# Optimization experiments

Measured on AMD Instinct MI355X. Metric: run time of the kernel, lower is better.

## Reference

```python
import jax, jax.numpy as jnp
import numpy as np

GROUP_SIZES = (64, 128, 256, 96, 160, 224, 192, 288, 320, 112, 80, 48, 32, 16, 32)
LENGTH = 512
ALPHABET = 21


def setup_inputs() -> dict:
    key = jax.random.key(0)
    keys = jax.random.split(key, len(GROUP_SIZES) + 1)
    n_samples = int(sum(GROUP_SIZES))
    inp = {"x": jax.random.normal(keys[0], (n_samples, LENGTH, ALPHABET), dtype=jnp.float32)}
    for i, g in enumerate(GROUP_SIZES):
        inp[f"mat{i}"] = jax.random.normal(keys[i + 1], (g, g), dtype=jnp.float32)
    return inp


def reference(x, mat0, mat1, mat2, mat3, mat4, mat5, mat6, mat7, mat8, mat9,
              mat10, mat11, mat12, mat13, mat14):
    mats = (mat0, mat1, mat2, mat3, mat4, mat5, mat6, mat7, mat8, mat9,
            mat10, mat11, mat12, mat13, mat14)
    # Block-diagonal grouped matmul along the sample dim: out[sl] = mats_i @ x[sl].
    # Group boundaries are static Python ints, so slicing is jit-friendly.
    pieces = []
    start = 0
    for m, g in zip(mats, GROUP_SIZES):
        xg = x[start:start + g]  # (g, L, A)
        pieces.append(jnp.einsum('gh,hla->gla', m, xg))
        start += g
    return jnp.concatenate(pieces, axis=0)
```

## Files before the change

### kernel.cpp

```cpp
#include <hip/hip_runtime.h>
#include <hip/hip_bf16.h>

#define NCOL 10752
#define NROW 2048
#define NG 15
#define NTILES 23

typedef __bf16 bf16;
typedef __attribute__((ext_vector_type(8))) __bf16 bf16x8;
typedef __attribute__((ext_vector_type(4))) __bf16 bf16x4;
typedef __attribute__((ext_vector_type(4))) float f32x4;

__constant__ int c_gsize[NG]  = {64,128,256,96,160,224,192,288,320,112,80,48,32,16,32};
__constant__ int c_gstart[NG] = {0,64,192,448,544,704,928,1120,1408,1728,1840,1920,1968,2000,2016};
__constant__ int c_tgrp[NTILES] = {8,8,8,7,7,7,2,2,5,5,6,6,4,4,1,9,3,10,0,11,12,14,13};
__constant__ int c_trow[NTILES] = {0,128,256,0,128,256,0,128,0,128,0,128,0,128,0,0,0,0,0,0,0,0,0};

struct MatPtrs { const float* p[NG]; };

constexpr int BM = 128, BN = 128, BK = 32, BKp = 40;

__global__ __launch_bounds__(256)
void matapply_kernel(const float* __restrict__ x, MatPtrs mats, float* __restrict__ out)
{
    __shared__ bf16 sA[2][BM][BKp];
    __shared__ bf16 sB[2][BN][BKp];

    const int tid    = threadIdx.x;
    const int colb   = blockIdx.x * BN;
    const int tileid = blockIdx.y;

    const int grp  = c_tgrp[tileid];
    const int row0 = c_trow[tileid];
    const int g    = c_gsize[grp];
    const int s    = c_gstart[grp];
    const float* __restrict__ M = mats.p[grp];

    const int wave = tid >> 6;
    const int lane = tid & 63;
    const int wr   = (wave & 1) * 64;
    const int wc   = (wave >> 1) * 64;
    const int lm   = lane & 15;
    const int kq   = lane >> 4;
    const int kb   = kq * 8;

    const int aK = (tid & 7) * 4;
    const int aR = tid >> 3;
    const int bC = (tid & 31) * 4;
    const int bK = (tid >> 5) * 4;

    const int nIter = (g + BK - 1) / BK;

    f32x4 acc[4][4];
    #pragma unroll
    for (int i = 0; i < 4; i++)
        #pragma unroll
        for (int j = 0; j < 4; j++)
            acc[i][j] = (f32x4){0.f, 0.f, 0.f, 0.f};

    float4 av[4], xv[4];

    #pragma unroll
    for (int i = 0; i < 4; i++) {
        int r = aR + 32 * i;
        av[i] = make_float4(0.f, 0.f, 0.f, 0.f);
        if ((row0 + r) < g && aK < g)
            av[i] = *(const float4*)(M + (size_t)(row0 + r) * g + aK);
    }
    #pragma unroll
    for (int j = 0; j < 4; j++)
        xv[j] = *(const float4*)(x + (size_t)(s + bK + j) * NCOL + colb + bC);

    #pragma unroll
    for (int i = 0; i < 4; i++) {
        int r = aR + 32 * i;
        bf16x4 w;
        w[0] = (bf16)av[i].x; w[1] = (bf16)av[i].y; w[2] = (bf16)av[i].z; w[3] = (bf16)av[i].w;
        *(bf16x4*)&sA[0][r][aK] = w;
    }
    #pragma unroll
    for (int cc = 0; cc < 4; cc++) {
        int lc = bC + cc;
        bf16x4 w;
        #pragma unroll
        for (int j = 0; j < 4; j++)
            w[j] = (bf16)(((const float*)&xv[j])[cc]);
        *(bf16x4*)&sB[0][lc][bK ^ (((lc >> 2) & 3) << 3)] = w;
    }
    __syncthreads();

    for (int it = 0; it < nIter; ++it) {
        const int cur = it & 1;
        const bool more = (it + 1) < nIter;

        if (more) {
            const int k0 = (it + 1) * BK;
            #pragma unroll
            for (int i = 0; i < 4; i++) {
                int r = aR + 32 * i;
                av[i] = make_float4(0.f, 0.f, 0.f, 0.f);
                if ((row0 + r) < g && (k0 + aK) < g)
                    av[i] = *(const float4*)(M + (size_t)(row0 + r) * g + (k0 + aK));
            }
            #pragma unroll
            for (int j = 0; j < 4; j++)
                xv[j] = *(const float4*)(x + (size_t)(s + k0 + bK + j) * NCOL + colb + bC);
        }

        bf16x8 af[4], bfr[4];
        #pragma unroll
        for (int i = 0; i < 4; i++)
            af[i] = *(const bf16x8*)&sA[cur][wr + i * 16 + lm][kb];
        #pragma unroll
        for (int j = 0; j < 4; j++) {
            int lc = wc + j * 16 + lm;
            bfr[j] = *(const bf16x8*)&sB[cur][lc][kb ^ (((lc >> 2) & 3) << 3)];
        }
        #pragma unroll
        for (int i = 0; i < 4; i++)
            #pragma unroll
            for (int j = 0; j < 4; j++)
                acc[i][j] = __builtin_amdgcn_mfma_f32_16x16x32_bf16(af[i], bfr[j], acc[i][j], 0, 0, 0);

        if (more) {
            const int nxt = 1 - cur;
            #pragma unroll
            for (int i = 0; i < 4; i++) {
                int r = aR + 32 * i;
                bf16x4 w;
                w[0] = (bf16)av[i].x; w[1] = (bf16)av[i].y; w[2] = (bf16)av[i].z; w[3] = (bf16)av[i].w;
                *(bf16x4*)&sA[nxt][r][aK] = w;
            }
            #pragma unroll
            for (int cc = 0; cc < 4; cc++) {
                int lc = bC + cc;
                bf16x4 w;
                #pragma unroll
                for (int j = 0; j < 4; j++)
                    w[j] = (bf16)(((const float*)&xv[j])[cc]);
                *(bf16x4*)&sB[nxt][lc][bK ^ (((lc >> 2) & 3) << 3)] = w;
            }
            __syncthreads();
        }
    }

    #pragma unroll
    for (int i = 0; i < 4; i++) {
        #pragma unroll
        for (int r = 0; r < 4; r++) {
            int row = row0 + wr + i * 16 + kq * 4 + r;
            if (row < g) {
                float* orow = out + (size_t)(s + row) * NCOL + colb + wc;
                #pragma unroll
                for (int j = 0; j < 4; j++)
                    orow[j * 16 + lm] = acc[i][j][r];
            }
        }
    }
}

extern "C" void kernel_launch(void* const* d_in, const int* in_sizes, int n_in,
                              void* d_out, int out_size, void* d_ws, size_t ws_size,
                              hipStream_t stream)
{
    const float* x = (const float*)d_in[0];
    MatPtrs mp;
    for (int i = 0; i < NG; i++) mp.p[i] = (const float*)d_in[1 + i];
    float* out = (float*)d_out;

    dim3 grid(NCOL / BN, NTILES);
    dim3 block(256);
    matapply_kernel<<<grid, block, 0, stream>>>(x, mp, out);
}
```

Measured before the change: 192.4 us.

## Shrink GEMM tiles to 64x64 with finer row tiling and new LDS swizzles

Block tiles drop from 128x128 to 64x64, and the row-tile table is rebuilt at 64-row granularity, giving 37 row tiles and a grid four times larger. The aim is less padding waste on groups whose size is not a multiple of 128, plus better occupancy, declared through launch bounds of 6 blocks. New XOR swizzles are applied to the A and B shared-memory tiles to cut bank conflicts. In exchange, each loaded tile is reused across fewer outputs, there are more block launches and barriers per unit of work, and the B stores to shared memory become narrower bf16x2 writes.

```diff
diff --git a/kernel.cpp b/kernel.cpp
--- a/kernel.cpp
+++ b/kernel.cpp
@@ -1,30 +1,36 @@
 #include <hip/hip_runtime.h>
-#include <hip/hip_bf16.h>
 
 #define NCOL 10752
-#define NROW 2048
 #define NG 15
-#define NTILES 23
+#define NTILES 37
 
 typedef __bf16 bf16;
 typedef __attribute__((ext_vector_type(8))) __bf16 bf16x8;
 typedef __attribute__((ext_vector_type(4))) __bf16 bf16x4;
+typedef __attribute__((ext_vector_type(2))) __bf16 bf16x2;
 typedef __attribute__((ext_vector_type(4))) float f32x4;
 
 __constant__ int c_gsize[NG]  = {64,128,256,96,160,224,192,288,320,112,80,48,32,16,32};
 __constant__ int c_gstart[NG] = {0,64,192,448,544,704,928,1120,1408,1728,1840,1920,1968,2000,2016};
-__constant__ int c_tgrp[NTILES] = {8,8,8,7,7,7,2,2,5,5,6,6,4,4,1,9,3,10,0,11,12,14,13};
-__constant__ int c_trow[NTILES] = {0,128,256,0,128,256,0,128,0,128,0,128,0,128,0,0,0,0,0,0,0,0,0};
+__constant__ int c_tgrp[NTILES] = {8,8,8,8,8, 7,7,7,7,7, 2,2,2,2, 5,5,5,5, 6,6,6, 4,4,4, 1,1, 9,9, 3,3, 10,10, 0, 11, 12, 13, 14};
+__constant__ int c_trow[NTILES] = {0,64,128,192,256, 0,64,128,192,256, 0,64,128,192, 0,64,128,192, 0,64,128, 0,64,128, 0,64, 0,64, 0,64, 0,64, 0, 0, 0, 0, 0};
 
 struct MatPtrs { const float* p[NG]; };
 
-constexpr int BM = 128, BN = 128, BK = 32, BKp = 40;
+constexpr int BM = 64, BN = 64, BK = 32, BKp = 40;
 
-__global__ __launch_bounds__(256)
+__device__ __forceinline__ int swzB(int lc, int k) {
+    return k ^ ((((lc >> 2) ^ (lc >> 4)) & 3) << 3);
+}
+__device__ __forceinline__ int swzA(int r, int k) {
+    return k ^ (((r >> 1) & 3) << 3);
+}
+
+__global__ __launch_bounds__(256, 6)
 void matapply_kernel(const float* __restrict__ x, MatPtrs mats, float* __restrict__ out)
 {
-    __shared__ bf16 sA[2][BM][BKp];
-    __shared__ bf16 sB[2][BN][BKp];
+    __shared__ __align__(16) bf16 sA[2][BM][BKp];
+    __shared__ __align__(16) bf16 sB[2][BN][BKp];
 
     const int tid    = threadIdx.x;
     const int colb   = blockIdx.x * BN;
@@ -38,54 +44,53 @@
 
     const int wave = tid >> 6;
     const int lane = tid & 63;
-    const int wr   = (wave & 1) * 64;
-    const int wc   = (wave >> 1) * 64;
+    const int wr   = (wave & 1) * 32;
+    const int wc   = (wave >> 1) * 32;
     const int lm   = lane & 15;
     const int kq   = lane >> 4;
     const int kb   = kq * 8;
 
     const int aK = (tid & 7) * 4;
     const int aR = tid >> 3;
-    const int bC = (tid & 31) * 4;
-    const int bK = (tid >> 5) * 4;
+    const int bC = (tid & 15) * 4;
+    const int bK = (tid >> 4) * 2;
 
     const int nIter = (g + BK - 1) / BK;
 
-    f32x4 acc[4][4];
+    f32x4 acc[2][2];
     #pragma unroll
-    for (int i = 0; i < 4; i++)
+    for (int i = 0; i < 2; i++)
         #pragma unroll
-        for (int j = 0; j < 4; j++)
+        for (int j = 0; j < 2; j++)
             acc[i][j] = (f32x4){0.f, 0.f, 0.f, 0.f};
 
-    float4 av[4], xv[4];
+    float4 av[2], xv[2];
 
     #pragma unroll
-    for (int i = 0; i < 4; i++) {
+    for (int i = 0; i < 2; i++) {
         int r = aR + 32 * i;
         av[i] = make_float4(0.f, 0.f, 0.f, 0.f);
         if ((row0 + r) < g && aK < g)
             av[i] = *(const float4*)(M + (size_t)(row0 + r) * g + aK);
     }
     #pragma unroll
-    for (int j = 0; j < 4; j++)
+    for (int j = 0; j < 2; j++)
         xv[j] = *(const float4*)(x + (size_t)(s + bK + j) * NCOL + colb + bC);
 
     #pragma unroll
-    for (int i = 0; i < 4; i++) {
+    for (int i = 0; i < 2; i++) {
         int r = aR + 32 * i;
         bf16x4 w;
         w[0] = (bf16)av[i].x; w[1] = (bf16)av[i].y; w[2] = (bf16)av[i].z; w[3] = (bf16)av[i].w;
-        *(bf16x4*)&sA[0][r][aK] = w;
+        *(bf16x4*)&sA[0][r][swzA(r, aK)] = w;
     }
     #pragma unroll
     for (int cc = 0; cc < 4; cc++) {
         int lc = bC + cc;
-        bf16x4 w;
-        #pragma unroll
-        for (int j = 0; j < 4; j++)
-            w[j] = (bf16)(((const float*)&xv[j])[cc]);
-        *(bf16x4*)&sB[0][lc][bK ^ (((lc >> 2) & 3) << 3)] = w;
+        bf16x2 w;
+        w[0] = (bf16)(((const float*)&xv[0])[cc]);
+        w[1] = (bf16)(((const float*)&xv[1])[cc]);
+        *(bf16x2*)&sB[0][lc][swzB(lc, bK)] = w;
     }
     __syncthreads();
 
@@ -96,64 +101,64 @@
         if (more) {
             const int k0 = (it + 1) * BK;
             #pragma unroll
-            for (int i = 0; i < 4; i++) {
+            for (int i = 0; i < 2; i++) {
                 int r = aR + 32 * i;
                 av[i] = make_float4(0.f, 0.f, 0.f, 0.f);
                 if ((row0 + r) < g && (k0 + aK) < g)
-                    av[i] = *(const float4*)(M + (size_t)(row0 + r) * g + (k0 + aK));
+                    av[i] = *(const float4*)(M + (size_t)(row0 + r) * g + k0 + aK);
             }
             #pragma unroll
-            for (int j = 0; j < 4; j++)
+            for (int j = 0; j < 2; j++)
                 xv[j] = *(const float4*)(x + (size_t)(s + k0 + bK + j) * NCOL + colb + bC);
         }
 
-        bf16x8 af[4], bfr[4];
+        bf16x8 af[2], bfr[2];
         #pragma unroll
-        for (int i = 0; i < 4; i++)
-            af[i] = *(const bf16x8*)&sA[cur][wr + i * 16 + lm][kb];
-        #pragma unroll
-        for (int j = 0; j < 4; j++) {
-            int lc = wc + j * 16 + lm;
-            bfr[j] = *(const bf16x8*)&sB[cur][lc][kb ^ (((lc >> 2) & 3) << 3)];
+        for (int i = 0; i < 2; i++) {
+            int r = wr + 16 * i + lm;
+            af[i] = *(const bf16x8*)&sA[cur][r][swzA(r, kb)];
         }
         #pragma unroll
-        for (int i = 0; i < 4; i++)
+        for (int j = 0; j < 2; j++) {
+            int lc = wc + 16 * j + lm;
+            bfr[j] = *(const bf16x8*)&sB[cur][lc][swzB(lc, kb)];
+        }
+        #pragma unroll
+        for (int i = 0; i < 2; i++)
             #pragma unroll
-            for (int j = 0; j < 4; j++)
+            for (int j = 0; j < 2; j++)
                 acc[i][j] = __builtin_amdgcn_mfma_f32_16x16x32_bf16(af[i], bfr[j], acc[i][j], 0, 0, 0);
 
         if (more) {
             const int nxt = 1 - cur;
             #pragma unroll
-            for (int i = 0; i < 4; i++) {
+            for (int i = 0; i < 2; i++) {
                 int r = aR + 32 * i;
                 bf16x4 w;
                 w[0] = (bf16)av[i].x; w[1] = (bf16)av[i].y; w[2] = (bf16)av[i].z; w[3] = (bf16)av[i].w;
-                *(bf16x4*)&sA[nxt][r][aK] = w;
+                *(bf16x4*)&sA[nxt][r][swzA(r, aK)] = w;
             }
             #pragma unroll
             for (int cc = 0; cc < 4; cc++) {
                 int lc = bC + cc;
-                bf16x4 w;
-                #pragma unroll
-                for (int j = 0; j < 4; j++)
-                    w[j] = (bf16)(((const float*)&xv[j])[cc]);
-                *(bf16x4*)&sB[nxt][lc][bK ^ (((lc >> 2) & 3) << 3)] = w;
+                bf16x2 w;
+                w[0] = (bf16)(((const float*)&xv[0])[cc]);
+                w[1] = (bf16)(((const float*)&xv[1])[cc]);
+                *(bf16x2*)&sB[nxt][lc][swzB(lc, bK)] = w;
             }
             __syncthreads();
         }
     }
 
     #pragma unroll
-    for (int i = 0; i < 4; i++) {
+    for (int i = 0; i < 2; i++) {
         #pragma unroll
         for (int r = 0; r < 4; r++) {
-            int row = row0 + wr + i * 16 + kq * 4 + r;
+            int row = row0 + wr + 16 * i + kq * 4 + r;
             if (row < g) {
                 float* orow = out + (size_t)(s + row) * NCOL + colb + wc;
-                #pragma unroll
-                for (int j = 0; j < 4; j++)
-                    orow[j * 16 + lm] = acc[i][j][r];
+                orow[lm]      = acc[i][0][r];
+                orow[16 + lm] = acc[i][1][r];
             }
         }
     }
```

Result: slower. 204.0 us (+6.0%).

## Pre-pack weight tiles to bf16 MFMA layout and stream via global_load_lds

Applied to the files above, without the earlier changes.

A new prep kernel converts each group's weight matrix into bf16 tiles laid out in MFMA fragment order in workspace memory. The main kernel then loads the A tiles straight into LDS with global_load_lds, skipping the per-block fp32 load, conversion and LDS writes of the weights. This is meant to cut redundant weight conversion across the 84 column blocks and to ease register pressure (launch bounds now request 4 blocks). The cost is an extra kernel launch and a dependency on workspace size, with the old kernel kept as a fallback.

```diff
diff --git a/kernel.cpp b/kernel.cpp
--- a/kernel.cpp
+++ b/kernel.cpp
@@ -1,10 +1,9 @@
 #include <hip/hip_runtime.h>
-#include <hip/hip_bf16.h>
 
 #define NCOL 10752
-#define NROW 2048
 #define NG 15
 #define NTILES 23
+#define WS_NEED 1064960
 
 typedef __bf16 bf16;
 typedef __attribute__((ext_vector_type(8))) __bf16 bf16x8;
@@ -13,17 +12,48 @@
 
 __constant__ int c_gsize[NG]  = {64,128,256,96,160,224,192,288,320,112,80,48,32,16,32};
 __constant__ int c_gstart[NG] = {0,64,192,448,544,704,928,1120,1408,1728,1840,1920,1968,2000,2016};
-__constant__ int c_tgrp[NTILES] = {8,8,8,7,7,7,2,2,5,5,6,6,4,4,1,9,3,10,0,11,12,14,13};
-__constant__ int c_trow[NTILES] = {0,128,256,0,128,256,0,128,0,128,0,128,0,128,0,0,0,0,0,0,0,0,0};
+__constant__ int c_tgrp[NTILES]  = {8,8,8,7,7,7,2,2,5,5,6,6,4,4,1,9,3,10,0,11,12,14,13};
+__constant__ int c_trow[NTILES]  = {0,128,256,0,128,256,0,128,0,128,0,128,0,128,0,0,0,0,0,0,0,0,0};
+__constant__ int c_niter[NTILES] = {10,10,10,9,9,9,8,8,7,7,6,6,5,5,4,4,3,3,2,2,1,1,1};
+__constant__ int c_tbase[NTILES] = {0,10,20,30,39,48,57,65,73,80,87,93,99,104,109,113,117,120,123,125,127,128,129};
 
 struct MatPtrs { const float* p[NG]; };
 
 constexpr int BM = 128, BN = 128, BK = 32, BKp = 40;
 
 __global__ __launch_bounds__(256)
-void matapply_kernel(const float* __restrict__ x, MatPtrs mats, float* __restrict__ out)
+void prep_kernel(MatPtrs mats, bf16* __restrict__ ws)
 {
-    __shared__ bf16 sA[2][BM][BKp];
+    const int kt = blockIdx.x, tile = blockIdx.y;
+    if (kt >= c_niter[tile]) return;
+    const int grp  = c_tgrp[tile];
+    const int row0 = c_trow[tile];
+    const int g    = c_gsize[grp];
+    const float* __restrict__ M = mats.p[grp];
+    bf16* dst = ws + (size_t)(c_tbase[tile] + kt) * 4096;
+
+    #pragma unroll
+    for (int h = 0; h < 2; h++) {
+        const int u    = threadIdx.x + h * 256;
+        const int l    = u & 63;
+        const int st   = u >> 6;
+        const int row  = row0 + st * 16 + (l & 15);
+        const int kcol = kt * 32 + (l >> 4) * 8;
+        bf16x8 w = {};
+        if (row < g && kcol < g) {
+            const float* src = M + (size_t)row * g + kcol;
+            #pragma unroll
+            for (int j = 0; j < 8; j++) w[j] = (bf16)src[j];
+        }
+        *(bf16x8*)(dst + (size_t)u * 8) = w;
+    }
+}
+
+__global__ __launch_bounds__(256, 4)
+void matapply_kernel(const float* __restrict__ x, const bf16* __restrict__ aws,
+                     float* __restrict__ out)
+{
+    __shared__ bf16 sA[2][4096];
     __shared__ bf16 sB[2][BN][BKp];
 
     const int tid    = threadIdx.x;
@@ -31,10 +61,10 @@
     const int tileid = blockIdx.y;
 
     const int grp  = c_tgrp[tileid];
-    const int row0 = c_trow[tileid];
     const int g    = c_gsize[grp];
     const int s    = c_gstart[grp];
-    const float* __restrict__ M = mats.p[grp];
+    const int row0 = c_trow[tileid];
+    const bf16* __restrict__ aimg = aws + (size_t)c_tbase[tileid] * 4096;
 
     const int wave = tid >> 6;
     const int lane = tid & 63;
@@ -44,6 +74,126 @@
     const int kq   = lane >> 4;
     const int kb   = kq * 8;
 
+    const int bC = (tid & 31) * 4;
+    const int bK = (tid >> 5) * 4;
+
+    const int nIter = (g + BK - 1) / BK;
+
+    f32x4 acc[4][4];
+    #pragma unroll
+    for (int i = 0; i < 4; i++)
+        #pragma unroll
+        for (int j = 0; j < 4; j++)
+            acc[i][j] = (f32x4){0.f, 0.f, 0.f, 0.f};
+
+    float4 xv[4];
+
+    auto glds_a = [&](int buf, int kt) {
+        const bf16* src = aimg + (size_t)kt * 4096 + (size_t)(wave * 2) * 512 + lane * 8;
+        #pragma unroll
+        for (int c = 0; c < 2; c++)
+            __builtin_amdgcn_global_load_lds(
+                (const __attribute__((address_space(1))) unsigned int*)(src + c * 512),
+                (__attribute__((address_space(3))) unsigned int*)&sA[buf][(wave * 2 + c) * 512],
+                16, 0, 0);
+    };
+
+    glds_a(0, 0);
+    #pragma unroll
+    for (int j = 0; j < 4; j++)
+        xv[j] = *(const float4*)(x + (size_t)(s + bK + j) * NCOL + colb + bC);
+    #pragma unroll
+    for (int cc = 0; cc < 4; cc++) {
+        int lc = bC + cc;
+        bf16x4 w;
+        #pragma unroll
+        for (int j = 0; j < 4; j++)
+            w[j] = (bf16)(((const float*)&xv[j])[cc]);
+        *(bf16x4*)&sB[0][lc][bK ^ (((lc >> 2) & 3) << 3)] = w;
+    }
+    __syncthreads();
+
+    for (int it = 0; it < nIter; ++it) {
+        const int cur = it & 1;
+        const bool more = (it + 1) < nIter;
+
+        if (more) {
+            glds_a(1 - cur, it + 1);
+            const int k0 = (it + 1) * BK;
+            #pragma unroll
+            for (int j = 0; j < 4; j++)
+                xv[j] = *(const float4*)(x + (size_t)(s + k0 + bK + j) * NCOL + colb + bC);
+        }
+
+        bf16x8 af[4], bfr[4];
+        #pragma unroll
+        for (int i = 0; i < 4; i++)
+            af[i] = *(const bf16x8*)&sA[cur][((wave & 1) * 4 + i) * 512 + lane * 8];
+        #pragma unroll
+        for (int j = 0; j < 4; j++) {
+            int lc = wc + j * 16 + lm;
+            bfr[j] = *(const bf16x8*)&sB[cur][lc][kb ^ (((lc >> 2) & 3) << 3)];
+        }
+        #pragma unroll
+        for (int i = 0; i < 4; i++)
+            #pragma unroll
+            for (int j = 0; j < 4; j++)
+                acc[i][j] = __builtin_amdgcn_mfma_f32_16x16x32_bf16(af[i], bfr[j], acc[i][j], 0, 0, 0);
+
+        if (more) {
+            const int nxt = 1 - cur;
+            #pragma unroll
+            for (int cc = 0; cc < 4; cc++) {
+                int lc = bC + cc;
+                bf16x4 w;
+                #pragma unroll
+                for (int j = 0; j < 4; j++)
+                    w[j] = (bf16)(((const float*)&xv[j])[cc]);
+                *(bf16x4*)&sB[nxt][lc][bK ^ (((lc >> 2) & 3) << 3)] = w;
+            }
+            __syncthreads();
+        }
+    }
+
+    #pragma unroll
+    for (int i = 0; i < 4; i++) {
+        #pragma unroll
+        for (int r = 0; r < 4; r++) {
+            int row = row0 + wr + i * 16 + kq * 4 + r;
+            if (row < g) {
+                float* orow = out + (size_t)(s + row) * NCOL + colb + wc;
+                #pragma unroll
+                for (int j = 0; j < 4; j++)
+                    orow[j * 16 + lm] = acc[i][j][r];
+            }
+        }
+    }
+}
+
+__global__ __launch_bounds__(256)
+void matapply_fb(const float* __restrict__ x, MatPtrs mats, float* __restrict__ out)
+{
+    __shared__ bf16 sA[2][BM][BKp];
+    __shared__ bf16 sB[2][BN][BKp];
+
+    const int tid    = threadIdx.x;
+    const int colb   = blockIdx.x * BN;
+    const int tileid = blockIdx.y;
+
+    const int grp  = c_tgrp[tileid];
+    const int row0 = c_trow[tileid];
+    const int g    = c_gsize[grp];
+    const int s    = c_gstart[grp];
+    const float* __restrict__ M = mats.p[grp];
+
+    const int wave = tid >> 6;
+    const int lane = tid & 63;
+    const int wr   = (wave & 1) * 64;
+    const int wc   = (wave >> 1) * 64;
+    const int lm   = lane & 15;
+    const int kq   = lane >> 4;
+    const int kb   = kq * 8;
+
     const int aK = (tid & 7) * 4;
     const int aR = tid >> 3;
     const int bC = (tid & 31) * 4;
@@ -100,7 +250,7 @@
                 int r = aR + 32 * i;
                 av[i] = make_float4(0.f, 0.f, 0.f, 0.f);
                 if ((row0 + r) < g && (k0 + aK) < g)
-                    av[i] = *(const float4*)(M + (size_t)(row0 + r) * g + (k0 + aK));
+                    av[i] = *(const float4*)(M + (size_t)(row0 + r) * g + k0 + aK);
             }
             #pragma unroll
             for (int j = 0; j < 4; j++)
@@ -168,7 +318,11 @@
     for (int i = 0; i < NG; i++) mp.p[i] = (const float*)d_in[1 + i];
     float* out = (float*)d_out;
 
-    dim3 grid(NCOL / BN, NTILES);
-    dim3 block(256);
-    matapply_kernel<<<grid, block, 0, stream>>>(x, mp, out);
+    if (d_ws != nullptr && ws_size >= (size_t)WS_NEED) {
+        prep_kernel<<<dim3(10, NTILES), dim3(256), 0, stream>>>(mp, (bf16*)d_ws);
+        matapply_kernel<<<dim3(NCOL / BN, NTILES), dim3(256), 0, stream>>>(
+            x, (const bf16*)d_ws, out);
+    } else {
+        matapply_fb<<<dim3(NCOL / BN, NTILES), dim3(256), 0, stream>>>(x, mp, out);
+    }
 }
```

After: 192.8 us. About the same (+0.2%).

## Pre-pack bf16 matrix fragments and use 64-row tiles with per-wave LDS

Applied to the files above, without the earlier changes.

Adds a prep kernel that converts each group matrix to bf16 in MFMA fragment order in the workspace. The main kernel switches to 64-row tiles (37 tiles instead of 23), so smaller groups waste less padded work. Each wave reads A fragments straight from global memory and stages only its own 32-column B slice in private LDS, which removes block-wide __syncthreads. The costs are an extra launch, re-reading x for each 64-row tile instead of each 128-row tile, and a fallback path kept for when no workspace is supplied.

```diff
diff --git a/kernel.cpp b/kernel.cpp
--- a/kernel.cpp
+++ b/kernel.cpp
@@ -1,10 +1,10 @@
 #include <hip/hip_runtime.h>
-#include <hip/hip_bf16.h>
 
 #define NCOL 10752
-#define NROW 2048
 #define NG 15
-#define NTILES 23
+#define NT37 37
+#define NT23 23
+#define WS_NEED 913408
 
 typedef __bf16 bf16;
 typedef __attribute__((ext_vector_type(8))) __bf16 bf16x8;
@@ -13,25 +13,154 @@
 
 __constant__ int c_gsize[NG]  = {64,128,256,96,160,224,192,288,320,112,80,48,32,16,32};
 __constant__ int c_gstart[NG] = {0,64,192,448,544,704,928,1120,1408,1728,1840,1920,1968,2000,2016};
-__constant__ int c_tgrp[NTILES] = {8,8,8,7,7,7,2,2,5,5,6,6,4,4,1,9,3,10,0,11,12,14,13};
-__constant__ int c_trow[NTILES] = {0,128,256,0,128,256,0,128,0,128,0,128,0,128,0,0,0,0,0,0,0,0,0};
+
+__constant__ int t37_grp[NT37]  = {8,8,8,8,8, 7,7,7,7,7, 2,2,2,2, 5,5,5,5, 6,6,6, 4,4,4, 1,1, 9,9, 3,3, 10,10, 0, 11, 12, 14, 13};
+__constant__ int t37_row[NT37]  = {0,64,128,192,256, 0,64,128,192,256, 0,64,128,192, 0,64,128,192, 0,64,128, 0,64,128, 0,64, 0,64, 0,64, 0,64, 0, 0, 0, 0, 0};
+__constant__ int t37_kn[NT37]   = {10,10,10,10,10, 9,9,9,9,9, 8,8,8,8, 7,7,7,7, 6,6,6, 5,5,5, 4,4, 4,4, 3,3, 3,3, 2, 2, 1, 1, 1};
+__constant__ int t37_base[NT37] = {0,10,20,30,40, 50,59,68,77,86, 95,103,111,119, 127,134,141,148, 155,161,167, 173,178,183, 188,192, 196,200, 204,207, 210,213, 216, 218, 220, 221, 222};
+
+__constant__ int t23_grp[NT23] = {8,8,8,7,7,7,2,2,5,5,6,6,4,4,1,9,3,10,0,11,12,14,13};
+__constant__ int t23_row[NT23] = {0,128,256,0,128,256,0,128,0,128,0,128,0,128,0,0,0,0,0,0,0,0,0};
 
 struct MatPtrs { const float* p[NG]; };
 
-constexpr int BM = 128, BN = 128, BK = 32, BKp = 40;
+constexpr int BKp = 40;
+
+__device__ __forceinline__ int bkey(int col) { return ((col >> 2) & 3) << 3; }
 
 __global__ __launch_bounds__(256)
-void matapply_kernel(const float* __restrict__ x, MatPtrs mats, float* __restrict__ out)
+void prep_kernel(MatPtrs mats, bf16* __restrict__ ws)
 {
-    __shared__ bf16 sA[2][BM][BKp];
-    __shared__ bf16 sB[2][BN][BKp];
+    const int kt = blockIdx.x, tile = blockIdx.y;
+    if (kt >= t37_kn[tile]) return;
+    const int grp  = t37_grp[tile];
+    const int row0 = t37_row[tile];
+    const int g    = c_gsize[grp];
+    const float* __restrict__ M = mats.p[grp];
+    bf16* dst = ws + (size_t)(t37_base[tile] + kt) * 2048;
+
+    const int u    = threadIdx.x;
+    const int l    = u & 63;
+    const int st   = u >> 6;
+    const int row  = row0 + st * 16 + (l & 15);
+    const int kcol = kt * 32 + (l >> 4) * 8;
+    bf16x8 w = {};
+    if (row < g && kcol < g) {
+        const float* src = M + (size_t)row * g + kcol;
+        #pragma unroll
+        for (int j = 0; j < 8; j++) w[j] = (bf16)src[j];
+    }
+    *(bf16x8*)(dst + (size_t)u * 8) = w;
+}
+
+__global__ __launch_bounds__(256, 5)
+void matapply_kernel(const float* __restrict__ x, const bf16* __restrict__ aws,
+                     float* __restrict__ out)
+{
+    __shared__ bf16 sB[4][2][32 * BKp];
 
     const int tid    = threadIdx.x;
-    const int colb   = blockIdx.x * BN;
+    const int colb   = blockIdx.x * 128;
     const int tileid = blockIdx.y;
 
-    const int grp  = c_tgrp[tileid];
-    const int row0 = c_trow[tileid];
+    const int grp  = t37_grp[tileid];
+    const int g    = c_gsize[grp];
+    const int s    = c_gstart[grp];
+    const int row0 = t37_row[tileid];
+    const int nIter = t37_kn[tileid];
+    const bf16* __restrict__ aimg = aws + (size_t)t37_base[tileid] * 2048;
+
+    const int wave = tid >> 6;
+    const int lane = tid & 63;
+    const int wc   = wave * 32;
+    const int lm   = lane & 15;
+    const int kq   = lane >> 4;
+    const int kb   = kq * 8;
+
+    const int bC = (lane & 7) * 4;
+    const int bK = (lane >> 3) * 4;
+
+    const float* __restrict__ xbase = x + (size_t)(s + bK) * NCOL + colb + wc + bC;
+    bf16* __restrict__ sBw0 = &sB[wave][0][0];
+    bf16* __restrict__ sBw1 = &sB[wave][1][0];
+
+    f32x4 acc[4][2];
+    #pragma unroll
+    for (int i = 0; i < 4; i++) {
+        acc[i][0] = (f32x4){0.f, 0.f, 0.f, 0.f};
+        acc[i][1] = (f32x4){0.f, 0.f, 0.f, 0.f};
+    }
+
+    float4 xv[4];
+    #pragma unroll
+    for (int q = 0; q < 4; q++)
+        xv[q] = *(const float4*)(xbase + (size_t)q * NCOL);
+
+    for (int it = 0; it < nIter; ++it) {
+        bf16* __restrict__ sBw = (it & 1) ? sBw1 : sBw0;
+
+        #pragma unroll
+        for (int cc = 0; cc < 4; cc++) {
+            const int col = bC + cc;
+            bf16x4 w;
+            w[0] = (bf16)xv[0][cc]; w[1] = (bf16)xv[1][cc];
+            w[2] = (bf16)xv[2][cc]; w[3] = (bf16)xv[3][cc];
+            *(bf16x4*)&sBw[col * BKp + (bK ^ bkey(col))] = w;
+        }
+
+        if (it + 1 < nIter) {
+            const size_t roff = (size_t)(it + 1) * 32;
+            #pragma unroll
+            for (int q = 0; q < 4; q++)
+                xv[q] = *(const float4*)(xbase + (roff + q) * NCOL);
+        }
+
+        bf16x8 av[4];
+        const bf16* ai = aimg + (size_t)it * 2048 + lane * 8;
+        #pragma unroll
+        for (int i = 0; i < 4; i++)
+            av[i] = *(const bf16x8*)(ai + i * 512);
+
+        bf16x8 bfr[2];
+        #pragma unroll
+        for (int j = 0; j < 2; j++) {
+            const int col = j * 16 + lm;
+            bfr[j] = *(const bf16x8*)&sBw[col * BKp + (kb ^ bkey(col))];
+        }
+
+        #pragma unroll
+        for (int i = 0; i < 4; i++) {
+            acc[i][0] = __builtin_amdgcn_mfma_f32_16x16x32_bf16(av[i], bfr[0], acc[i][0], 0, 0, 0);
+            acc[i][1] = __builtin_amdgcn_mfma_f32_16x16x32_bf16(av[i], bfr[1], acc[i][1], 0, 0, 0);
+        }
+    }
+
+    #pragma unroll
+    for (int i = 0; i < 4; i++) {
+        #pragma unroll
+        for (int r = 0; r < 4; r++) {
+            const int row = row0 + i * 16 + kq * 4 + r;
+            if (row < g) {
+                float* orow = out + (size_t)(s + row) * NCOL + colb + wc;
+                orow[lm]      = acc[i][0][r];
+                orow[16 + lm] = acc[i][1][r];
+            }
+        }
+    }
+}
+
+__global__ __launch_bounds__(256)
+void matapply_fb(const float* __restrict__ x, MatPtrs mats, float* __restrict__ out)
+{
+    __shared__ bf16 sAf[2][128][BKp];
+    __shared__ bf16 sBf[2][128][BKp];
+
+    const int tid    = threadIdx.x;
+    const int colb   = blockIdx.x * 128;
+    const int tileid = blockIdx.y;
+
+    const int grp  = t23_grp[tileid];
+    const int row0 = t23_row[tileid];
     const int g    = c_gsize[grp];
     const int s    = c_gstart[grp];
     const float* __restrict__ M = mats.p[grp];
@@ -49,7 +178,7 @@
     const int bC = (tid & 31) * 4;
     const int bK = (tid >> 5) * 4;
 
-    const int nIter = (g + BK - 1) / BK;
+    const int nIter = (g + 31) / 32;
 
     f32x4 acc[4][4];
     #pragma unroll
@@ -76,7 +205,7 @@
         int r = aR + 32 * i;
         bf16x4 w;
         w[0] = (bf16)av[i].x; w[1] = (bf16)av[i].y; w[2] = (bf16)av[i].z; w[3] = (bf16)av[i].w;
-        *(bf16x4*)&sA[0][r][aK] = w;
+        *(bf16x4*)&sAf[0][r][aK] = w;
     }
     #pragma unroll
     for (int cc = 0; cc < 4; cc++) {
@@ -85,7 +214,7 @@
         #pragma unroll
         for (int j = 0; j < 4; j++)
             w[j] = (bf16)(((const float*)&xv[j])[cc]);
-        *(bf16x4*)&sB[0][lc][bK ^ (((lc >> 2) & 3) << 3)] = w;
+        *(bf16x4*)&sBf[0][lc][bK ^ (((lc >> 2) & 3) << 3)] = w;
     }
     __syncthreads();
 
@@ -94,13 +223,13 @@
         const bool more = (it + 1) < nIter;
 
         if (more) {
-            const int k0 = (it + 1) * BK;
+            const int k0 = (it + 1) * 32;
             #pragma unroll
             for (int i = 0; i < 4; i++) {
                 int r = aR + 32 * i;
                 av[i] = make_float4(0.f, 0.f, 0.f, 0.f);
                 if ((row0 + r) < g && (k0 + aK) < g)
-                    av[i] = *(const float4*)(M + (size_t)(row0 + r) * g + (k0 + aK));
+                    av[i] = *(const float4*)(M + (size_t)(row0 + r) * g + k0 + aK);
             }
             #pragma unroll
             for (int j = 0; j < 4; j++)
@@ -110,11 +239,11 @@
         bf16x8 af[4], bfr[4];
         #pragma unroll
         for (int i = 0; i < 4; i++)
-            af[i] = *(const bf16x8*)&sA[cur][wr + i * 16 + lm][kb];
+            af[i] = *(const bf16x8*)&sAf[cur][wr + i * 16 + lm][kb];
         #pragma unroll
         for (int j = 0; j < 4; j++) {
             int lc = wc + j * 16 + lm;
-            bfr[j] = *(const bf16x8*)&sB[cur][lc][kb ^ (((lc >> 2) & 3) << 3)];
+            bfr[j] = *(const bf16x8*)&sBf[cur][lc][kb ^ (((lc >> 2) & 3) << 3)];
         }
         #pragma unroll
         for (int i = 0; i < 4; i++)
@@ -129,7 +258,7 @@
                 int r = aR + 32 * i;
                 bf16x4 w;
                 w[0] = (bf16)av[i].x; w[1] = (bf16)av[i].y; w[2] = (bf16)av[i].z; w[3] = (bf16)av[i].w;
-                *(bf16x4*)&sA[nxt][r][aK] = w;
+                *(bf16x4*)&sAf[nxt][r][aK] = w;
             }
             #pragma unroll
             for (int cc = 0; cc < 4; cc++) {
@@ -138,7 +267,7 @@
                 #pragma unroll
                 for (int j = 0; j < 4; j++)
                     w[j] = (bf16)(((const float*)&xv[j])[cc]);
-                *(bf16x4*)&sB[nxt][lc][bK ^ (((lc >> 2) & 3) << 3)] = w;
+                *(bf16x4*)&sBf[nxt][lc][bK ^ (((lc >> 2) & 3) << 3)] = w;
             }
             __syncthreads();
         }
@@ -168,7 +297,11 @@
     for (int i = 0; i < NG; i++) mp.p[i] = (const float*)d_in[1 + i];
     float* out = (float*)d_out;
 
-    dim3 grid(NCOL / BN, NTILES);
-    dim3 block(256);
-    matapply_kernel<<<grid, block, 0, stream>>>(x, mp, out);
+    if (d_ws != nullptr && ws_size >= (size_t)WS_NEED) {
+        prep_kernel<<<dim3(10, NT37), dim3(256), 0, stream>>>(mp, (bf16*)d_ws);
+        matapply_kernel<<<dim3(NCOL / 128, NT37), dim3(256), 0, stream>>>(
+            x, (const bf16*)d_ws, out);
+    } else {
+        matapply_fb<<<dim3(NCOL / 128, NT23), dim3(256), 0, stream>>>(x, mp, out);
+    }
 }
```

After: 206.6 us. 1.07x slower.
